# Performance work log

Hardware: AMD Instinct MI355X
Metric: run time of the kernel (lower is better)

Reference implementation:

```python
import jax, jax.numpy as jnp
import numpy as np

OUT_F, IN_F = 16384, 4096
TOKENS = 8192
PALETTE = 256


def setup_inputs() -> dict:
    key = jax.random.key(0)
    k1, k2, k3, k4 = jax.random.split(key, 4)
    input = jax.random.normal(k1, (TOKENS, IN_F), dtype=jnp.float32)
    weight_idx = jax.random.randint(k2, (OUT_F, IN_F), 0, PALETTE, dtype=jnp.int32)
    lookup_table = jax.random.normal(k3, (PALETTE,), dtype=jnp.float32)
    bias = jax.random.normal(k4, (OUT_F,), dtype=jnp.float32)
    return {"input": input, "weight_idx": weight_idx, "lookup_table": lookup_table, "bias": bias}


def reference(input, weight_idx, lookup_table, bias):
    # Dequantize: LUT gather expands uint8 indices to full-precision weights [out, in]
    full_weights = lookup_table[weight_idx]
    # F.linear: y = x @ W^T + b
    return jnp.einsum('ti,oi->to', input, full_weights) + bias
```

## Files before the change

### kernel.cpp

```cpp
#include <hip/hip_runtime.h>
#include <stdint.h>

#define TOKENS 8192
#define OUT_F  16384
#define IN_F   4096

typedef short bf16x8  __attribute__((ext_vector_type(8)));
typedef float f32x4   __attribute__((ext_vector_type(4)));
typedef float f32x16  __attribute__((ext_vector_type(16)));

__device__ __forceinline__ unsigned short bf16_rne(float f) {
    union { float f; unsigned int u; } v; v.f = f;
    unsigned int u = v.u;
    u += 0x7fffu + ((u >> 16) & 1u);
    return (unsigned short)(u >> 16);
}

__device__ __forceinline__ unsigned int pack_bf16x2(float a, float b) {
    return (unsigned int)bf16_rne(a) | ((unsigned int)bf16_rne(b) << 16);
}

__device__ __forceinline__ void async_cp16(const void* gptr, void* ldsptr) {
    __builtin_amdgcn_global_load_lds(
        (const __attribute__((address_space(1))) unsigned int*)gptr,
        (__attribute__((address_space(3))) unsigned int*)ldsptr,
        16, 0, 0);
}

__global__ __launch_bounds__(256) void cvt_input_kernel(
    const float* __restrict__ in, unsigned short* __restrict__ out, int n8)
{
    int i = blockIdx.x * 256 + threadIdx.x;
    if (i >= n8) return;
    size_t base = (size_t)i * 8;
    float4 a = *(const float4*)(in + base);
    float4 b = *(const float4*)(in + base + 4);
    uint4 p;
    p.x = pack_bf16x2(a.x, a.y);  p.y = pack_bf16x2(a.z, a.w);
    p.z = pack_bf16x2(b.x, b.y);  p.w = pack_bf16x2(b.z, b.w);
    *(uint4*)(out + base) = p;
}

__global__ __launch_bounds__(256) void dequant_kernel(
    const int* __restrict__ idx, const float* __restrict__ lut,
    unsigned short* __restrict__ out, int n8)
{
    __shared__ float slut[256];
    slut[threadIdx.x] = lut[threadIdx.x];
    __syncthreads();
    int i = blockIdx.x * 256 + threadIdx.x;
    if (i >= n8) return;
    size_t base = (size_t)i * 8;
    int4 i0 = *(const int4*)(idx + base);
    int4 i1 = *(const int4*)(idx + base + 4);
    uint4 p;
    p.x = pack_bf16x2(slut[i0.x], slut[i0.y]);
    p.y = pack_bf16x2(slut[i0.z], slut[i0.w]);
    p.z = pack_bf16x2(slut[i1.x], slut[i1.y]);
    p.w = pack_bf16x2(slut[i1.z], slut[i1.w]);
    *(uint4*)(out + base) = p;
}

__global__ __launch_bounds__(512, 2) void palett_gemm256(
    const unsigned short* __restrict__ A,
    const unsigned short* __restrict__ B,
    const float* __restrict__ bias,
    float* __restrict__ out)
{
    __shared__ __align__(16) char sm[131072];

    const int t    = threadIdx.x;
    const int w    = t >> 6;
    const int l    = t & 63;
    const int l31  = l & 31;
    const int hi   = l >> 5;
    const int wr   = w >> 2;
    const int wc   = w & 3;

    const int orig = blockIdx.y * gridDim.x + blockIdx.x;
    const int swzb = (orig & 7) * 256 + (orig >> 3);
    const int n0   = (swzb & 63) << 8;
    const int m0   = (swzb >> 6) << 8;

    const int srow = w * 16 + (l >> 3);
    const int scol = ((l & 7) ^ (l >> 3)) << 3;
    const unsigned short* pA = A + (size_t)(m0 + srow) * IN_F + scol;
    const unsigned short* pB = B + (size_t)(n0 + srow) * IN_F + scol;

    const int arow  = l31 * 128;
    const int bcol  = ((hi ^ (l & 7)) << 4);
    const int abase = wr * 16384;
    const int bbase = 32768 + (wc >> 1) * 16384 + (wc & 1) * 8192;

    f32x16 acc[4][2] = {};
    bf16x8 fA[2][4], fB[2][2];

#define STAGE(P, HOFF, LOFF, KOFF) do {                                          \
    async_cp16((P) + (size_t)(HOFF) * IN_F + (KOFF), sm + (LOFF) + w * 2048);    \
    async_cp16((P) + (size_t)((HOFF) + 8) * IN_F + (KOFF),                       \
               sm + (LOFF) + w * 2048 + 1024);                                   \
} while (0)

#define READ_K(S_, RB_, KK_) do {                                                \
    _Pragma("unroll")                                                            \
    for (int m_ = 0; m_ < 4; ++m_)                                               \
        fA[S_][m_] = *(const bf16x8*)(sm + (RB_) + abase + m_ * 4096 + arow      \
                                      + (((KK_) * 32) ^ bcol));                  \
    _Pragma("unroll")                                                            \
    for (int n_ = 0; n_ < 2; ++n_)                                               \
        fB[S_][n_] = *(const bf16x8*)(sm + (RB_) + bbase + n_ * 4096 + arow      \
                                      + (((KK_) * 32) ^ bcol));                  \
} while (0)

#define MFMA_K(S_) do {                                                          \
    __builtin_amdgcn_s_setprio(1);                                               \
    _Pragma("unroll")                                                            \
    for (int m_ = 0; m_ < 4; ++m_) {                                             \
        _Pragma("unroll")                                                        \
        for (int n_ = 0; n_ < 2; ++n_)                                           \
            acc[m_][n_] = __builtin_amdgcn_mfma_f32_32x32x16_bf16(               \
                fA[S_][m_], fB[S_][n_], acc[m_][n_], 0, 0, 0);                   \
    }                                                                            \
    __builtin_amdgcn_s_setprio(0);                                               \
} while (0)

#define TILE(RB_, WB_, KB_, KA_) do {                                            \
    READ_K(0, RB_, 0);                                                           \
    STAGE(pB, 0,   (WB_) + 32768, KB_);                                          \
    READ_K(1, RB_, 1);                                                           \
    MFMA_K(0);                                      \
    STAGE(pB, 128, (WB_) + 49152, KB_);                                          \
    READ_K(0, RB_, 2);                                                           \
    MFMA_K(1);                                                         \
    READ_K(1, RB_, 3);                                                           \
    MFMA_K(0);                                                         \
    asm volatile("s_waitcnt lgkmcnt(0)" ::: "memory");    \
    asm volatile("s_barrier" ::: "memory");                \
    STAGE(pA, 0,   (RB_) + 0,     KA_);                                          \
    STAGE(pA, 128, (RB_) + 16384, KA_);                                          \
    MFMA_K(1);                                                         \
    asm volatile("s_waitcnt vmcnt(4)" ::: "memory");       \
    asm volatile("s_barrier" ::: "memory");                       \
} while (0)

    STAGE(pA, 0,   0,             0);
    STAGE(pA, 128, 16384,         0);
    STAGE(pB, 0,   32768,         0);
    STAGE(pB, 128, 49152,         0);
    STAGE(pA, 0,   65536 + 0,     64);
    STAGE(pA, 128, 65536 + 16384, 64);
    asm volatile("s_waitcnt vmcnt(4)" ::: "memory");
    asm volatile("s_barrier" ::: "memory");

#pragma unroll 1
    for (int it = 0; it < 32; ++it) {
        const int tt  = 2 * it;
        const int kB0 = ((tt + 1) & 63) * 64;
        const int kA0 = ((tt + 2) & 63) * 64;
        const int kB1 = ((tt + 2) & 63) * 64;
        const int kA1 = ((tt + 3) & 63) * 64;
        TILE(0,     65536, kB0, kA0);
        TILE(65536, 0,     kB1, kA1);
    }
    asm volatile("s_waitcnt vmcnt(0)" ::: "memory");

#undef TILE
#undef MFMA_K
#undef READ_K
#undef STAGE

    float bj[2];
#pragma unroll
    for (int nj = 0; nj < 2; ++nj) bj[nj] = bias[n0 + wc * 64 + nj * 32 + l31];

#pragma unroll
    for (int mi = 0; mi < 4; ++mi) {
        const int mrow = m0 + wr * 128 + mi * 32 + hi * 4;
#pragma unroll
        for (int nj = 0; nj < 2; ++nj) {
            const int n = n0 + wc * 64 + nj * 32 + l31;
#pragma unroll
            for (int g = 0; g < 4; ++g) {
#pragma unroll
                for (int v = 0; v < 4; ++v) {
                    out[(size_t)(mrow + g * 8 + v) * OUT_F + n] =
                        acc[mi][nj][g * 4 + v] + bj[nj];
                }
            }
        }
    }
}

__global__ __launch_bounds__(256) void palett_gemm_fused(
    const float* __restrict__ Af,
    const int* __restrict__ Widx,
    const float* __restrict__ lut,
    const float* __restrict__ bias,
    float* __restrict__ out)
{
    __shared__ __align__(16) unsigned short smA[128 * 32];
    __shared__ __align__(16) unsigned short smB[128 * 32];
    __shared__ float slut[256];

    const int t    = threadIdx.x;
    const int w    = t >> 6;
    const int l    = t & 63;
    const int quad = l >> 4;
    const int r16  = l & 15;
    const int wr   = w >> 1;
    const int wc   = w & 1;

    const int m0 = blockIdx.y * 128;
    const int n0 = blockIdx.x * 128;

    const int g0  = t * 8;
    const int row = g0 >> 5;
    const int col = g0 & 31;

    char* const smA_c = (char*)smA;
    char* const smB_c = (char*)smB;

    slut[t] = lut[t];
    __syncthreads();

    uint32_t aoff[4], boff[4];
#pragma unroll
    for (int i = 0; i < 4; ++i) {
        aoff[i] = (uint32_t)(((wr * 64 + i * 16 + r16) * 32 + quad * 8) * 2);
        boff[i] = (uint32_t)(((wc * 64 + i * 16 + r16) * 32 + quad * 8) * 2);
    }

    f32x4 acc[4][4] = {};

    const float* af0 = Af + (size_t)(m0 + row) * IN_F + col;
    const float* af1 = Af + (size_t)(m0 + row + 64) * IN_F + col;
    const int*   wi0 = Widx + (size_t)(n0 + row) * IN_F + col;
    const int*   wi1 = Widx + (size_t)(n0 + row + 64) * IN_F + col;

    for (int k0 = 0; k0 < IN_F; k0 += 32) {
        float4 x0 = *(const float4*)(af0 + k0);
        float4 x1 = *(const float4*)(af0 + k0 + 4);
        uint4 p;
        p.x = pack_bf16x2(x0.x, x0.y); p.y = pack_bf16x2(x0.z, x0.w);
        p.z = pack_bf16x2(x1.x, x1.y); p.w = pack_bf16x2(x1.z, x1.w);
        *(uint4*)(smA_c + t * 16) = p;
        x0 = *(const float4*)(af1 + k0);
        x1 = *(const float4*)(af1 + k0 + 4);
        p.x = pack_bf16x2(x0.x, x0.y); p.y = pack_bf16x2(x0.z, x0.w);
        p.z = pack_bf16x2(x1.x, x1.y); p.w = pack_bf16x2(x1.z, x1.w);
        *(uint4*)(smA_c + 4096 + t * 16) = p;

        int4 j0 = *(const int4*)(wi0 + k0);
        int4 j1 = *(const int4*)(wi0 + k0 + 4);
        p.x = pack_bf16x2(slut[j0.x], slut[j0.y]);
        p.y = pack_bf16x2(slut[j0.z], slut[j0.w]);
        p.z = pack_bf16x2(slut[j1.x], slut[j1.y]);
        p.w = pack_bf16x2(slut[j1.z], slut[j1.w]);
        *(uint4*)(smB_c + t * 16) = p;
        j0 = *(const int4*)(wi1 + k0);
        j1 = *(const int4*)(wi1 + k0 + 4);
        p.x = pack_bf16x2(slut[j0.x], slut[j0.y]);
        p.y = pack_bf16x2(slut[j0.z], slut[j0.w]);
        p.z = pack_bf16x2(slut[j1.x], slut[j1.y]);
        p.w = pack_bf16x2(slut[j1.z], slut[j1.w]);
        *(uint4*)(smB_c + 4096 + t * 16) = p;
        __syncthreads();

        bf16x8 afr[4], bfr[4];
#pragma unroll
        for (int i = 0; i < 4; ++i) afr[i] = *(const bf16x8*)(smA_c + aoff[i]);
#pragma unroll
        for (int j = 0; j < 4; ++j) bfr[j] = *(const bf16x8*)(smB_c + boff[j]);
#pragma unroll
        for (int i = 0; i < 4; ++i)
#pragma unroll
            for (int j = 0; j < 4; ++j)
                acc[i][j] = __builtin_amdgcn_mfma_f32_16x16x32_bf16(
                    afr[i], bfr[j], acc[i][j], 0, 0, 0);
        __syncthreads();
    }

    float bj[4];
#pragma unroll
    for (int j = 0; j < 4; ++j) bj[j] = bias[n0 + wc * 64 + j * 16 + r16];

#pragma unroll
    for (int i = 0; i < 4; ++i) {
        const int mbase = m0 + wr * 64 + i * 16 + quad * 4;
#pragma unroll
        for (int j = 0; j < 4; ++j) {
            const int n = n0 + wc * 64 + j * 16 + r16;
#pragma unroll
            for (int v = 0; v < 4; ++v) {
                out[(size_t)(mbase + v) * OUT_F + n] = acc[i][j][v] + bj[j];
            }
        }
    }
}

extern "C" void kernel_launch(void* const* d_in, const int* in_sizes, int n_in,
                              void* d_out, int out_size, void* d_ws, size_t ws_size,
                              hipStream_t stream) {
    const float* input = (const float*)d_in[0];
    const int*   widx  = (const int*)d_in[1];
    const float* lut   = (const float*)d_in[2];
    const float* bias  = (const float*)d_in[3];
    float* out = (float*)d_out;

    const size_t aBytes = (size_t)TOKENS * IN_F * sizeof(unsigned short);
    const size_t bBytes = (size_t)OUT_F  * IN_F * sizeof(unsigned short);

    if (ws_size >= aBytes + bBytes) {
        unsigned short* wsA = (unsigned short*)d_ws;
        unsigned short* wsB = (unsigned short*)((char*)d_ws + aBytes);
        const int nA8 = (TOKENS * IN_F) / 8;
        const int nB8 = (OUT_F  * IN_F) / 8;
        cvt_input_kernel<<<(nA8 + 255) / 256, 256, 0, stream>>>(input, wsA, nA8);
        dequant_kernel<<<(nB8 + 255) / 256, 256, 0, stream>>>(widx, lut, wsB, nB8);
        dim3 grid2(OUT_F / 256, TOKENS / 256);
        palett_gemm256<<<grid2, 512, 0, stream>>>(wsA, wsB, bias, out);
    } else {
        dim3 grid(OUT_F / 128, TOKENS / 128);
        palett_gemm_fused<<<grid, 256, 0, stream>>>(input, widx, lut, bias, out);
    }
}
```

Measured before the change: 1.680 ms.

## Shrink GEMM block tile to 128x128 and switch to 16x16x32 MFMA

Replaces the 256x256-tile, 512-thread GEMM with a 128x128-tile, 256-thread kernel that uses 16x16x32 bf16 MFMAs, a 4x4 fragment grid per wave and 64KB of double-buffered LDS. The staging, swizzle and epilogue are rewritten to match the new layout, and the pipeline is simplified to two k-substeps per tile. The aim is more blocks in flight and a lighter LDS footprint, paid for with lower arithmetic intensity per block, meaning more global and LDS traffic per FLOP.

```diff
diff --git a/kernel.cpp b/kernel.cpp
--- a/kernel.cpp
+++ b/kernel.cpp
@@ -5,9 +5,8 @@
 #define OUT_F  16384
 #define IN_F   4096
 
-typedef short bf16x8  __attribute__((ext_vector_type(8)));
-typedef float f32x4   __attribute__((ext_vector_type(4)));
-typedef float f32x16  __attribute__((ext_vector_type(16)));
+typedef short bf16x8 __attribute__((ext_vector_type(8)));
+typedef float f32x4  __attribute__((ext_vector_type(4)));
 
 __device__ __forceinline__ unsigned short bf16_rne(float f) {
     union { float f; unsigned int u; } v; v.f = f;
@@ -61,96 +60,100 @@
     *(uint4*)(out + base) = p;
 }
 
-__global__ __launch_bounds__(512, 2) void palett_gemm256(
+__global__ __launch_bounds__(256, 2) void palett_gemm128(
     const unsigned short* __restrict__ A,
     const unsigned short* __restrict__ B,
     const float* __restrict__ bias,
     float* __restrict__ out)
 {
-    __shared__ __align__(16) char sm[131072];
+    __shared__ __align__(16) char sm[65536];
 
     const int t    = threadIdx.x;
     const int w    = t >> 6;
     const int l    = t & 63;
-    const int l31  = l & 31;
-    const int hi   = l >> 5;
-    const int wr   = w >> 2;
-    const int wc   = w & 3;
+    const int quad = l >> 4;
+    const int r16  = l & 15;
+    const int wr   = w >> 1;
+    const int wc   = w & 1;
 
     const int orig = blockIdx.y * gridDim.x + blockIdx.x;
-    const int swzb = (orig & 7) * 256 + (orig >> 3);
-    const int n0   = (swzb & 63) << 8;
-    const int m0   = (swzb >> 6) << 8;
-
-    const int srow = w * 16 + (l >> 3);
+    const int swzb = (orig & 7) * 1024 + (orig >> 3);
+    const int n0   = (swzb & 127) << 7;
+    const int m0   = (swzb >> 7) << 7;
+
+    const int srow = w * 8 + (l >> 3);
     const int scol = ((l & 7) ^ (l >> 3)) << 3;
     const unsigned short* pA = A + (size_t)(m0 + srow) * IN_F + scol;
     const unsigned short* pB = B + (size_t)(n0 + srow) * IN_F + scol;
 
-    const int arow  = l31 * 128;
-    const int bcol  = ((hi ^ (l & 7)) << 4);
-    const int abase = wr * 16384;
-    const int bbase = 32768 + (wc >> 1) * 16384 + (wc & 1) * 8192;
-
-    f32x16 acc[4][2] = {};
-    bf16x8 fA[2][4], fB[2][2];
-
-#define STAGE(P, HOFF, LOFF, KOFF) do {                                          \
-    async_cp16((P) + (size_t)(HOFF) * IN_F + (KOFF), sm + (LOFF) + w * 2048);    \
-    async_cp16((P) + (size_t)((HOFF) + 8) * IN_F + (KOFF),                       \
-               sm + (LOFF) + w * 2048 + 1024);                                   \
+    const int cswz = (r16 & 7) << 4;
+    int aRow[4], bRow[4];
+#pragma unroll
+    for (int i = 0; i < 4; ++i) {
+        aRow[i] = (wr * 64 + i * 16 + r16) * 128;
+        bRow[i] = 16384 + (wc * 64 + i * 16 + r16) * 128;
+    }
+
+    f32x4  acc[4][4] = {};
+    bf16x8 fA[2][4], fB[2][4];
+
+#define BAR()   asm volatile("s_barrier" ::: "memory")
+
+#define STAGE_A(LB, KOFF) do {                                                   \
+    _Pragma("unroll")                                                            \
+    for (int r_ = 0; r_ < 4; ++r_)                                               \
+        async_cp16(pA + (size_t)(r_ * 32) * IN_F + (KOFF),                       \
+                   sm + (LB) + r_ * 4096 + w * 1024);                            \
+} while (0)
+
+#define STAGE_B(LB, KOFF) do {                                                   \
+    _Pragma("unroll")                                                            \
+    for (int r_ = 0; r_ < 4; ++r_)                                               \
+        async_cp16(pB + (size_t)(r_ * 32) * IN_F + (KOFF),                       \
+                   sm + (LB) + 16384 + r_ * 4096 + w * 1024);                    \
 } while (0)
 
 #define READ_K(S_, RB_, KK_) do {                                                \
     _Pragma("unroll")                                                            \
-    for (int m_ = 0; m_ < 4; ++m_)                                               \
-        fA[S_][m_] = *(const bf16x8*)(sm + (RB_) + abase + m_ * 4096 + arow      \
-                                      + (((KK_) * 32) ^ bcol));                  \
-    _Pragma("unroll")                                                            \
-    for (int n_ = 0; n_ < 2; ++n_)                                               \
-        fB[S_][n_] = *(const bf16x8*)(sm + (RB_) + bbase + n_ * 4096 + arow      \
-                                      + (((KK_) * 32) ^ bcol));                  \
+    for (int i_ = 0; i_ < 4; ++i_)                                               \
+        fA[S_][i_] = *(const bf16x8*)(sm + (RB_) + aRow[i_]                      \
+                                      + ((((KK_) * 64) + quad * 16) ^ cswz));    \
+    _Pragma("unroll")                                                            \
+    for (int j_ = 0; j_ < 4; ++j_)                                               \
+        fB[S_][j_] = *(const bf16x8*)(sm + (RB_) + bRow[j_]                      \
+                                      + ((((KK_) * 64) + quad * 16) ^ cswz));    \
 } while (0)
 
 #define MFMA_K(S_) do {                                                          \
     __builtin_amdgcn_s_setprio(1);                                               \
     _Pragma("unroll")                                                            \
-    for (int m_ = 0; m_ < 4; ++m_) {                                             \
+    for (int i_ = 0; i_ < 4; ++i_) {                                             \
         _Pragma("unroll")                                                        \
-        for (int n_ = 0; n_ < 2; ++n_)                                           \
-            acc[m_][n_] = __builtin_amdgcn_mfma_f32_32x32x16_bf16(               \
-                fA[S_][m_], fB[S_][n_], acc[m_][n_], 0, 0, 0);                   \
+        for (int j_ = 0; j_ < 4; ++j_)                                           \
+            acc[i_][j_] = __builtin_amdgcn_mfma_f32_16x16x32_bf16(               \
+                fA[S_][i_], fB[S_][j_], acc[i_][j_], 0, 0, 0);                   \
     }                                                                            \
     __builtin_amdgcn_s_setprio(0);                                               \
 } while (0)
 
 #define TILE(RB_, WB_, KB_, KA_) do {                                            \
     READ_K(0, RB_, 0);                                                           \
-    STAGE(pB, 0,   (WB_) + 32768, KB_);                                          \
+    STAGE_B(WB_, KB_);                                                           \
     READ_K(1, RB_, 1);                                                           \
-    MFMA_K(0);                                      \
-    STAGE(pB, 128, (WB_) + 49152, KB_);                                          \
-    READ_K(0, RB_, 2);                                                           \
-    MFMA_K(1);                                                         \
-    READ_K(1, RB_, 3);                                                           \
-    MFMA_K(0);                                                         \
-    asm volatile("s_waitcnt lgkmcnt(0)" ::: "memory");    \
-    asm volatile("s_barrier" ::: "memory");                \
-    STAGE(pA, 0,   (RB_) + 0,     KA_);                                          \
-    STAGE(pA, 128, (RB_) + 16384, KA_);                                          \
-    MFMA_K(1);                                                         \
-    asm volatile("s_waitcnt vmcnt(4)" ::: "memory");       \
-    asm volatile("s_barrier" ::: "memory");                       \
-} while (0)
-
-    STAGE(pA, 0,   0,             0);
-    STAGE(pA, 128, 16384,         0);
-    STAGE(pB, 0,   32768,         0);
-    STAGE(pB, 128, 49152,         0);
-    STAGE(pA, 0,   65536 + 0,     64);
-    STAGE(pA, 128, 65536 + 16384, 64);
+    MFMA_K(0);                              \
+    asm volatile("s_waitcnt lgkmcnt(0)" ::: "memory");     \
+    BAR();                    \
+    STAGE_A(RB_, KA_);                                                           \
+    MFMA_K(1);                                                                   \
+    asm volatile("s_waitcnt vmcnt(4)" ::: "memory");        \
+    BAR();                                                                       \
+} while (0)
+
+    STAGE_A(0,     0);
+    STAGE_B(0,     0);
+    STAGE_A(32768, 64);
     asm volatile("s_waitcnt vmcnt(4)" ::: "memory");
-    asm volatile("s_barrier" ::: "memory");
+    BAR();
 
 #pragma unroll 1
     for (int it = 0; it < 32; ++it) {
@@ -159,34 +162,31 @@
         const int kA0 = ((tt + 2) & 63) * 64;
         const int kB1 = ((tt + 2) & 63) * 64;
         const int kA1 = ((tt + 3) & 63) * 64;
-        TILE(0,     65536, kB0, kA0);
-        TILE(65536, 0,     kB1, kA1);
+        TILE(0,     32768, kB0, kA0);
+        TILE(32768, 0,     kB1, kA1);
     }
     asm volatile("s_waitcnt vmcnt(0)" ::: "memory");
 
 #undef TILE
 #undef MFMA_K
 #undef READ_K
-#undef STAGE
-
-    float bj[2];
-#pragma unroll
-    for (int nj = 0; nj < 2; ++nj) bj[nj] = bias[n0 + wc * 64 + nj * 32 + l31];
-
-#pragma unroll
-    for (int mi = 0; mi < 4; ++mi) {
-        const int mrow = m0 + wr * 128 + mi * 32 + hi * 4;
-#pragma unroll
-        for (int nj = 0; nj < 2; ++nj) {
-            const int n = n0 + wc * 64 + nj * 32 + l31;
-#pragma unroll
-            for (int g = 0; g < 4; ++g) {
-#pragma unroll
-                for (int v = 0; v < 4; ++v) {
-                    out[(size_t)(mrow + g * 8 + v) * OUT_F + n] =
-                        acc[mi][nj][g * 4 + v] + bj[nj];
-                }
-            }
+#undef STAGE_B
+#undef STAGE_A
+#undef BAR
+
+    float bj[4];
+#pragma unroll
+    for (int j = 0; j < 4; ++j) bj[j] = bias[n0 + wc * 64 + j * 16 + r16];
+
+#pragma unroll
+    for (int mf = 0; mf < 4; ++mf) {
+        const int mrow = m0 + wr * 64 + mf * 16 + quad * 4;
+#pragma unroll
+        for (int nf = 0; nf < 4; ++nf) {
+            const int n = n0 + wc * 64 + nf * 16 + r16;
+#pragma unroll
+            for (int v = 0; v < 4; ++v)
+                out[(size_t)(mrow + v) * OUT_F + n] = acc[mf][nf][v] + bj[nf];
         }
     }
 }
@@ -317,8 +317,8 @@
         const int nB8 = (OUT_F  * IN_F) / 8;
         cvt_input_kernel<<<(nA8 + 255) / 256, 256, 0, stream>>>(input, wsA, nA8);
         dequant_kernel<<<(nB8 + 255) / 256, 256, 0, stream>>>(widx, lut, wsB, nB8);
-        dim3 grid2(OUT_F / 256, TOKENS / 256);
-        palett_gemm256<<<grid2, 512, 0, stream>>>(wsA, wsB, bias, out);
+        dim3 grid2(OUT_F / 128, TOKENS / 128);
+        palett_gemm128<<<grid2, 256, 0, stream>>>(wsA, wsB, bias, out);
     } else {
         dim3 grid(OUT_F / 128, TOKENS / 128);
         palett_gemm_fused<<<grid, 256, 0, stream>>>(input, widx, lut, bias, out);
```

After: 1.992 ms. +18.6%, slower.
